# Performance work log

Hardware: AMD Instinct MI355X
Metric: run time of the kernel (lower is better)

The kernel has to match this reference:

```python
import jax, jax.numpy as jnp
import numpy as np
from jax import lax

D = 256      # d_model
NH = 4       # nhead == len(multi_size)
DH = D // NH # per-head dim = 64
B, H, W = 8, 32, 32
EPS_LN = 1e-5
EPS_ATT = 1e-6


def conv2d(x, w, pad):
    # x: [B,C,H,W], w: [O,I,k,k], SAME padding via pad=k//2
    return lax.conv_general_dilated(
        x, w, window_strides=(1, 1), padding=[(pad, pad), (pad, pad)],
        dimension_numbers=("NCHW", "OIHW", "NCHW"))


def layer_norm(x, g, b):
    m = jnp.mean(x, axis=-1, keepdims=True)
    v = jnp.mean((x - m) ** 2, axis=-1, keepdims=True)
    return (x - m) * lax.rsqrt(v + EPS_LN) * g + b


def setup_inputs() -> dict:
    key = jax.random.key(0)
    ks = jax.random.split(key, 20)
    s = 0.02
    inp = {
        "x": jax.random.normal(ks[0], (B, D, H, W), jnp.float32),
        "source": jax.random.normal(ks[1], (B, D, H, W), jnp.float32),
        # q projection: conv3x3 d_model -> d_model (bias-free)
        "Wq": jax.random.normal(ks[2], (D, D, 3, 3), jnp.float32) * s,
        # MultiConv k projection: kernels 1,3,5,7, each d_model -> dim
        "Wk1": jax.random.normal(ks[3], (DH, D, 1, 1), jnp.float32) * s,
        "Wk3": jax.random.normal(ks[4], (DH, D, 3, 3), jnp.float32) * s,
        "Wk5": jax.random.normal(ks[5], (DH, D, 5, 5), jnp.float32) * s,
        "Wk7": jax.random.normal(ks[6], (DH, D, 7, 7), jnp.float32) * s,
        # MultiConv v projection
        "Wv1": jax.random.normal(ks[7], (DH, D, 1, 1), jnp.float32) * s,
        "Wv3": jax.random.normal(ks[8], (DH, D, 3, 3), jnp.float32) * s,
        "Wv5": jax.random.normal(ks[9], (DH, D, 5, 5), jnp.float32) * s,
        "Wv7": jax.random.normal(ks[10], (DH, D, 7, 7), jnp.float32) * s,
        # merge linear (bias=False), stored [in,out]
        "Wm": jax.random.normal(ks[11], (D, D), jnp.float32) * s,
        "ln1_g": jnp.ones((D,), jnp.float32),
        "ln1_b": jnp.zeros((D,), jnp.float32),
        "ln2_g": jnp.ones((D,), jnp.float32),
        "ln2_b": jnp.zeros((D,), jnp.float32),
        # FF mlp: Linear(2D->2D, no bias), ReLU, Linear(2D->D, no bias); [in,out]
        "W1": jax.random.normal(ks[12], (2 * D, 2 * D), jnp.float32) * s,
        "W2": jax.random.normal(ks[13], (2 * D, D), jnp.float32) * s,
    }
    return inp


def _forward(x, source, Wq, Wk1, Wk3, Wk5, Wk7, Wv1, Wv3, Wv5, Wv7,
             Wm, ln1_g, ln1_b, ln2_g, ln2_b, W1, W2):
    b, c, h, w = x.shape
    h1, w1 = source.shape[2], source.shape[3]
    L = h * w
    S = h1 * w1

    # projections (multi-scale convs -> heads along channel)
    q = conv2d(x, Wq, 1)                                        # [b,D,h,w]
    k = jnp.concatenate([conv2d(source, Wk1, 0), conv2d(source, Wk3, 1),
                         conv2d(source, Wk5, 2), conv2d(source, Wk7, 3)], axis=1)
    v = jnp.concatenate([conv2d(source, Wv1, 0), conv2d(source, Wv3, 1),
                         conv2d(source, Wv5, 2), conv2d(source, Wv7, 3)], axis=1)

    # b c h w -> b (h w) (nhead dim) -> b L nhead dim
    q = q.transpose(0, 2, 3, 1).reshape(b, L, NH, DH)
    k = k.transpose(0, 2, 3, 1).reshape(b, S, NH, DH)
    v = v.transpose(0, 2, 3, 1).reshape(b, S, NH, DH)

    # FullAttention_vis: softmax attention map [b, L, S, nhead]
    temp = DH ** -0.5
    qk = jnp.einsum("blhd,bshd->blsh", q, k)
    attn_vis = jax.nn.softmax(qk * temp, axis=2)

    # LinearAttention (elu+1 kernel feature map)
    Qf = jax.nn.elu(q) + 1.0
    Kf = jax.nn.elu(k) + 1.0
    v_len = jnp.float32(S)
    vals = v / v_len
    KV = jnp.einsum("bshd,bshv->bhdv", Kf, vals)                # [b,NH,DH,DH]
    Z = 1.0 / (jnp.einsum("blhd,bhd->blh", Qf, Kf.sum(axis=1)) + EPS_ATT)
    msg = jnp.einsum("blhd,bhdv,blh->blhv", Qf, KV, Z) * v_len  # [b,L,NH,DH]

    # merge + norm1
    msg = layer_norm(msg.reshape(b, L, D) @ Wm, ln1_g, ln1_b)

    # FF (mlp): cat -> Linear -> ReLU -> Linear -> norm2
    xf = x.transpose(0, 2, 3, 1).reshape(b, L, c)
    ff = jax.nn.relu(jnp.concatenate([xf, msg], axis=2) @ W1) @ W2
    msg = layer_norm(ff, ln2_g, ln2_b)                          # [b,L,D]
    msg = msg.reshape(b, h, w, c).transpose(0, 3, 1, 2)         # b c h w

    out = x + msg
    # b (h0 w0) (h1 w1) c -> b c h0 w0 h1 w1
    vis = attn_vis.reshape(b, h, w, h1, w1, NH).transpose(0, 5, 1, 2, 3, 4)
    return out, vis


def reference(x, source, Wq, Wk1, Wk3, Wk5, Wk7, Wv1, Wv3, Wv5, Wv7,
              Wm, ln1_g, ln1_b, ln2_g, ln2_b, W1, W2):
    return _forward(x, source, Wq, Wk1, Wk3, Wk5, Wk7, Wv1, Wv3, Wv5, Wv7,
                    Wm, ln1_g, ln1_b, ln2_g, ln2_b, W1, W2)
```

## Files before the change

kernel.cpp:

```cpp
#include <hip/hip_runtime.h>

#define DEV __device__ __forceinline__

typedef unsigned short u16;
typedef unsigned int u32;
typedef __bf16 bf16x8 __attribute__((ext_vector_type(8)));
typedef float f32x4 __attribute__((ext_vector_type(4)));

DEV float elu1(float x) { return x > 0.f ? x + 1.f : __expf(x); }

DEV u16 f2bf(float f) {
    union { float f; unsigned u; } v; v.f = f;
    unsigned r = v.u + 0x7fffu + ((v.u >> 16) & 1u);
    return (u16)(r >> 16);
}

__global__ __launch_bounds__(256) void repack_kernel(
    const float* __restrict__ Wq,
    const float* __restrict__ Wk1, const float* __restrict__ Wk3,
    const float* __restrict__ Wk5, const float* __restrict__ Wk7,
    const float* __restrict__ Wv1, const float* __restrict__ Wv3,
    const float* __restrict__ Wv5, const float* __restrict__ Wv7,
    u16* __restrict__ wpack)
{
    int gid = blockIdx.x * 256 + threadIdx.x;
    int frag = gid >> 6, l = gid & 63;
    const float* W; int K, ocbase = 0, rel;
    if (frag < 1152) {
        W = Wq; K = 3; int slot = frag / 288; rel = frag % 288; ocbase = slot * 64;
    } else {
        int f = frag - 1152; int side = f / 2688; f %= 2688;
        if (f < 32)        { W = side ? Wv1 : Wk1; K = 1; rel = f; }
        else if (f < 320)  { W = side ? Wv3 : Wk3; K = 3; rel = f - 32; }
        else if (f < 1120) { W = side ? Wv5 : Wk5; K = 5; rel = f - 320; }
        else               { W = side ? Wv7 : Wk7; K = 7; rel = f - 1120; }
    }
    int og = rel & 3, cc = (rel >> 2) & 7, tap = rel >> 5;
    int dy = tap / K, dx = tap % K;
    int oc = ocbase + og * 16 + (l & 15);
    int c0 = cc * 32 + (l >> 4) * 8;
    u16 pk[8];
#pragma unroll
    for (int j = 0; j < 8; ++j)
        pk[j] = f2bf(W[((size_t)(oc * 256 + c0 + j) * K + dy) * K + dx]);
    *(int4*)&wpack[(size_t)frag * 512 + l * 8] = *(const int4*)pk;
}

__global__ __launch_bounds__(256) void cast_src_kernel(
    const float* __restrict__ x, const float* __restrict__ src,
    u16* __restrict__ xbh, u16* __restrict__ sbh)
{
    __shared__ float lds[32 * 129];
    const int i = blockIdx.x, t = threadIdx.x;
    const int inp = i >> 9, rem = i & 511;
    const int b = rem >> 6, cc = (rem >> 3) & 7, pxb = rem & 7;
    const float* in = (inp ? src : x) + ((size_t)b * 256 + cc * 32) * 1024 + pxb * 128;
    u16* outp = (inp ? sbh : xbh) + (size_t)b * 262144 + (size_t)cc * 32768 + pxb * 128 * 32;
#pragma unroll
    for (int u = 0; u < 4; ++u) {
        int unit = t + u * 256;
        int r = unit >> 5, px4 = unit & 31;
        float4 v = *(const float4*)(in + (size_t)r * 1024 + px4 * 4);
        lds[r * 129 + px4 * 4 + 0] = v.x;
        lds[r * 129 + px4 * 4 + 1] = v.y;
        lds[r * 129 + px4 * 4 + 2] = v.z;
        lds[r * 129 + px4 * 4 + 3] = v.w;
    }
    __syncthreads();
#pragma unroll
    for (int u = 0; u < 2; ++u) {
        int unit = t + u * 256;
        int px = unit >> 2, cg = unit & 3;
        u16 pk[8];
#pragma unroll
        for (int j = 0; j < 8; ++j) pk[j] = f2bf(lds[(cg * 8 + j) * 129 + px]);
        *(int4*)&outp[px * 32 + cg * 8] = *(const int4*)pk;
    }
}

__global__ __launch_bounds__(256) void cast_qk_kernel(
    const float* __restrict__ qb, const float* __restrict__ kb,
    u16* __restrict__ qbt, u16* __restrict__ kbt)
{
    __shared__ float lds[64 * 65];
    const int i = blockIdx.x, t = threadIdx.x;
    const int inp = i >> 9, rem = i & 511;
    const int b = rem >> 6, h = (rem >> 4) & 3, pxb = rem & 15;
    const float* in = (inp ? kb : qb) + ((size_t)b * 256 + h * 64) * 1024 + pxb * 64;
    u16* outp = (inp ? kbt : qbt) + (((size_t)(b * 4 + h)) * 1024 + pxb * 64) * 64;
#pragma unroll
    for (int u = 0; u < 4; ++u) {
        int unit = t + u * 256;
        int r = unit >> 4, px4 = unit & 15;
        float4 v = *(const float4*)(in + (size_t)r * 1024 + px4 * 4);
        lds[r * 65 + px4 * 4 + 0] = v.x;
        lds[r * 65 + px4 * 4 + 1] = v.y;
        lds[r * 65 + px4 * 4 + 2] = v.z;
        lds[r * 65 + px4 * 4 + 3] = v.w;
    }
    __syncthreads();
#pragma unroll
    for (int u = 0; u < 2; ++u) {
        int unit = t + u * 256;
        int px = unit >> 3, cg = unit & 7;
        u16 pk[8];
#pragma unroll
        for (int j = 0; j < 8; ++j) pk[j] = f2bf(lds[(cg * 8 + j) * 65 + px]);
        *(int4*)&outp[px * 64 + cg * 8] = *(const int4*)pk;
    }
}

__global__ __launch_bounds__(256) void repack_ff_kernel(
    const float* __restrict__ W1, const float* __restrict__ W2,
    u16* __restrict__ w1p, u16* __restrict__ w2p)
{
    int gid = blockIdx.x * 256 + threadIdx.x;
    int f = gid >> 6, l = gid & 63;
    u16 pk[8];
    if (f < 512) {
        int ks = f >> 5, nf = f & 31;
#pragma unroll
        for (int j = 0; j < 8; ++j)
            pk[j] = f2bf(W1[(size_t)(ks * 32 + (l >> 4) * 8 + j) * 512 + nf * 16 + (l & 15)]);
        *(int4*)&w1p[(size_t)f * 512 + l * 8] = *(const int4*)pk;
    } else {
        int f2 = f - 512;
        int ks = f2 >> 4, nf = f2 & 15;
#pragma unroll
        for (int j = 0; j < 8; ++j)
            pk[j] = f2bf(W2[(size_t)(ks * 32 + (l >> 4) * 8 + j) * 256 + nf * 16 + (l & 15)]);
        *(int4*)&w2p[(size_t)f2 * 512 + l * 8] = *(const int4*)pk;
    }
}

template<int K>
DEV void conv_mfma_body(const u16* __restrict__ srcb,
                        const u16* __restrict__ wsec,
                        float* __restrict__ dst,
                        u16* Bt, int y0, int cch0, int ncc, int t)
{
    constexpr int P = K / 2;
    const int w = t >> 6, l = t & 63;
    const int chi = l >> 4, ln = l & 15;
    const int rowbase = chi * 22 + w * 2 + 3 - P;
    const int colbase = ln + 3 - P;
    f32x4 acc[4][4];
#pragma unroll
    for (int m = 0; m < 4; ++m)
#pragma unroll
        for (int n = 0; n < 4; ++n) acc[m][n] = (f32x4){0.f, 0.f, 0.f, 0.f};

    for (int cc = 0; cc < ncc; ++cc) {
        const int ccg = cch0 + cc;
        __syncthreads();
#pragma unroll
        for (int u = 0; u < 7; ++u) {
            int unit = t + (u << 9);
            if (unit < 2816) {
                int xv = unit & 31, r = unit >> 5;
                int yy = r % 22, ch = r / 22;
                int ygl = y0 - 3 + yy;
                int4 pk;
                if ((unsigned)ygl < 32u)
                    pk = *(const int4*)&srcb[(size_t)ccg * 32768 + (ygl * 32 + xv) * 32 + ch * 8];
                else
                    pk = (int4){0, 0, 0, 0};
                *(int4*)&Bt[((ch * 22 + yy) * 40 + xv + 3) * 8] = pk;
            } else if (unit < 3520) {
                int hu = unit - 2816;
                int hx = hu & 7; int xi = hx < 3 ? hx : hx + 32;
                int r = hu >> 3; int yy = r % 22, ch = r / 22;
                int4 z = {0, 0, 0, 0};
                *(int4*)&Bt[((ch * 22 + yy) * 40 + xi) * 8] = z;
            }
        }
        __syncthreads();
#pragma unroll
        for (int dy = 0; dy < K; ++dy) {
#pragma unroll
            for (int dx = 0; dx < K; ++dx) {
                const int tap = dy * K + dx;
                const u16* wp = wsec + ((size_t)(tap * 8 + ccg) * 4) * 512 + l * 8;
                bf16x8 a0 = *(const bf16x8*)(wp);
                bf16x8 a1 = *(const bf16x8*)(wp + 512);
                bf16x8 a2 = *(const bf16x8*)(wp + 1024);
                bf16x8 a3 = *(const bf16x8*)(wp + 1536);
                bf16x8 bf[4];
#pragma unroll
                for (int n = 0; n < 4; ++n) {
                    int row = rowbase + dy + (n >> 1);
                    int col = colbase + dx + (n & 1) * 16;
                    bf[n] = *(const bf16x8*)&Bt[(row * 40 + col) * 8];
                }
#pragma unroll
                for (int n = 0; n < 4; ++n) {
                    acc[0][n] = __builtin_amdgcn_mfma_f32_16x16x32_bf16(a0, bf[n], acc[0][n], 0, 0, 0);
                    acc[1][n] = __builtin_amdgcn_mfma_f32_16x16x32_bf16(a1, bf[n], acc[1][n], 0, 0, 0);
                    acc[2][n] = __builtin_amdgcn_mfma_f32_16x16x32_bf16(a2, bf[n], acc[2][n], 0, 0, 0);
                    acc[3][n] = __builtin_amdgcn_mfma_f32_16x16x32_bf16(a3, bf[n], acc[3][n], 0, 0, 0);
                }
            }
        }
    }
#pragma unroll
    for (int m = 0; m < 4; ++m)
#pragma unroll
        for (int n = 0; n < 4; ++n) {
            int y = y0 + w * 2 + (n >> 1);
            int px = y * 32 + (n & 1) * 16 + ln;
            int ocb = m * 16 + chi * 4;
#pragma unroll
            for (int r = 0; r < 4; ++r)
                dst[(size_t)(ocb + r) * 1024 + px] = acc[m][n][r];
        }
}

__global__ __launch_bounds__(512) void conv_mfma_kernel(
    const u16* __restrict__ xbh, const u16* __restrict__ sbh,
    const u16* __restrict__ wpack,
    float* __restrict__ qb, float* __restrict__ kb, float* __restrict__ vb,
    float* __restrict__ p5, float* __restrict__ p7)
{
    __shared__ u16 Bt[4 * 22 * 40 * 8];
    const int bx = blockIdx.x, t = threadIdx.x;
    const int b = bx >> 6, r = bx & 63;
    if (r < 8) {
        int slot = r >> 1, yt = r & 1;
        conv_mfma_body<3>(xbh + (size_t)b * 262144,
                          wpack + (size_t)(slot * 288) * 512,
                          qb + ((size_t)b * 256 + slot * 64) * 1024,
                          Bt, yt * 16, 0, 8, t);
        return;
    }
    const int r2 = r - 8;
    const int side = r2 / 28, r3 = r2 % 28;
    const u16* sp = sbh + (size_t)b * 262144;
    float* fin = side ? vb : kb;
    const size_t wkb = 1152 + (size_t)side * 2688;
    if (r3 < 2) {
        conv_mfma_body<1>(sp, wpack + (wkb + 0) * 512,
                          fin + ((size_t)b * 256) * 1024, Bt, r3 * 16, 0, 8, t);
    } else if (r3 < 4) {
        conv_mfma_body<3>(sp, wpack + (wkb + 32) * 512,
                          fin + ((size_t)b * 256 + 64) * 1024, Bt, (r3 - 2) * 16, 0, 8, t);
    } else if (r3 < 12) {
        int t5 = r3 - 4, cpart = t5 >> 1, yt = t5 & 1;
        conv_mfma_body<5>(sp, wpack + (wkb + 320) * 512,
                          p5 + (((size_t)side * 4 + cpart) * 8 + b) * 65536,
                          Bt, yt * 16, cpart * 2, 2, t);
    } else {
        int t7 = r3 - 12, cpart = t7 >> 1, yt = t7 & 1;
        conv_mfma_body<7>(sp, wpack + (wkb + 1120) * 512,
                          p7 + (((size_t)side * 8 + cpart) * 8 + b) * 65536,
                          Bt, yt * 16, cpart, 1, t);
    }
}

__global__ __launch_bounds__(256) void reduce_kernel(
    const float* __restrict__ p5, const float* __restrict__ p7,
    float* __restrict__ kb, float* __restrict__ vb)
{
    int gid = blockIdx.x * 256 + threadIdx.x;
    int px4 = gid & 255;
    int rr = gid >> 8;
    int oc = rr & 63, b = (rr >> 6) & 7, head = (rr >> 9) & 1, side = rr >> 10;
    float* outb = side ? vb : kb;
    float4 s = make_float4(0.f, 0.f, 0.f, 0.f);
    if (head == 0) {
#pragma unroll
        for (int p = 0; p < 4; ++p) {
            float4 u = *((const float4*)(p5 + (((size_t)side * 4 + p) * 8 + b) * 65536 + (size_t)oc * 1024) + px4);
            s.x += u.x; s.y += u.y; s.z += u.z; s.w += u.w;
        }
        *((float4*)(outb + ((size_t)b * 256 + 128 + oc) * 1024) + px4) = s;
    } else {
#pragma unroll
        for (int p = 0; p < 8; ++p) {
            float4 u = *((const float4*)(p7 + (((size_t)side * 8 + p) * 8 + b) * 65536 + (size_t)oc * 1024) + px4);
            s.x += u.x; s.y += u.y; s.z += u.z; s.w += u.w;
        }
        *((float4*)(outb + ((size_t)b * 256 + 192 + oc) * 1024) + px4) = s;
    }
}

__global__ __launch_bounds__(512) void qk_sm_kernel(const u16* __restrict__ qbt,
                                                    const u16* __restrict__ kbt,
                                                    float* __restrict__ vis)
{
    __shared__ u16 kf[32 * 512];
    __shared__ u16 qf[4 * 512];
    __shared__ float redM[32 * 8];
    __shared__ float redS[32 * 8];
    const int t = threadIdx.x;
    const int bx = blockIdx.x;
    const int b = bx >> 7, h = (bx >> 5) & 3, l0 = (bx & 31) * 32;
    const u16* qtp = qbt + ((size_t)(b * 4 + h)) * 1024 * 64;
    const u16* ktp = kbt + ((size_t)(b * 4 + h)) * 1024 * 64;

    if (t < 256) {
        int r = t & 31, dblk = t >> 5;
        int4 pk = *(const int4*)&qtp[(size_t)(l0 + r) * 64 + dblk * 8];
        *(int4*)&qf[(((r >> 4) * 2 + (dblk >> 2)) * 64 + (dblk & 3) * 16 + (r & 15)) * 8] = pk;
    }
    __syncthreads();

    const int w = t >> 6, l = t & 63, ln = l & 15, lg = l >> 4;
    bf16x8 a[2][2];
#pragma unroll
    for (int fr = 0; fr < 2; ++fr)
#pragma unroll
        for (int ks = 0; ks < 2; ++ks)
            a[fr][ks] = *(const bf16x8*)&qf[((fr * 2 + ks) * 64 + l) * 8];

    f32x4 acc[2][4][2];
#pragma unroll
    for (int fr = 0; fr < 2; ++fr)
#pragma unroll
        for (int cc = 0; cc < 4; ++cc)
#pragma unroll
            for (int f = 0; f < 2; ++f) acc[fr][cc][f] = (f32x4){0.f, 0.f, 0.f, 0.f};

#pragma unroll
    for (int cc = 0; cc < 4; ++cc) {
        __syncthreads();
#pragma unroll
        for (int it = 0; it < 4; ++it) {
            int unit = it * 512 + t;
            int sl = unit & 255, dblk = unit >> 8;
            int4 pk = *(const int4*)&ktp[(size_t)(cc * 256 + sl) * 64 + dblk * 8];
            *(int4*)&kf[(((sl >> 4) * 2 + (dblk >> 2)) * 64 + (dblk & 3) * 16 + (sl & 15)) * 8] = pk;
        }
        __syncthreads();
#pragma unroll
        for (int f = 0; f < 2; ++f) {
            int fg = (w * 2 + f) * 2;
            bf16x8 b0 = *(const bf16x8*)&kf[((fg + 0) * 64 + l) * 8];
            bf16x8 b1 = *(const bf16x8*)&kf[((fg + 1) * 64 + l) * 8];
#pragma unroll
            for (int fr = 0; fr < 2; ++fr) {
                acc[fr][cc][f] = __builtin_amdgcn_mfma_f32_16x16x32_bf16(a[fr][0], b0, acc[fr][cc][f], 0, 0, 0);
                acc[fr][cc][f] = __builtin_amdgcn_mfma_f32_16x16x32_bf16(a[fr][1], b1, acc[fr][cc][f], 0, 0, 0);
            }
        }
    }

#pragma unroll
    for (int fr = 0; fr < 2; ++fr)
#pragma unroll
        for (int cc = 0; cc < 4; ++cc)
#pragma unroll
            for (int f = 0; f < 2; ++f)
#pragma unroll
                for (int e = 0; e < 4; ++e) acc[fr][cc][f][e] *= 0.125f;

    float rmax[2][4];
#pragma unroll
    for (int fr = 0; fr < 2; ++fr)
#pragma unroll
        for (int reg = 0; reg < 4; ++reg) {
            float m = -1e30f;
#pragma unroll
            for (int cc = 0; cc < 4; ++cc)
#pragma unroll
                for (int f = 0; f < 2; ++f) m = fmaxf(m, acc[fr][cc][f][reg]);
#pragma unroll
            for (int off = 1; off < 16; off <<= 1) m = fmaxf(m, __shfl_xor(m, off));
            if (ln == 0) redM[(fr * 16 + lg * 4 + reg) * 8 + w] = m;
            rmax[fr][reg] = m;
        }
    __syncthreads();
#pragma unroll
    for (int fr = 0; fr < 2; ++fr)
#pragma unroll
        for (int reg = 0; reg < 4; ++reg) {
            int r = fr * 16 + lg * 4 + reg;
            float m = redM[r * 8];
#pragma unroll
            for (int ww = 1; ww < 8; ++ww) m = fmaxf(m, redM[r * 8 + ww]);
            rmax[fr][reg] = m;
        }
#pragma unroll
    for (int fr = 0; fr < 2; ++fr)
#pragma unroll
        for (int reg = 0; reg < 4; ++reg) {
            float s = 0.f;
            float m = rmax[fr][reg];
#pragma unroll
            for (int cc = 0; cc < 4; ++cc)
#pragma unroll
                for (int f = 0; f < 2; ++f) {
                    float e = __expf(acc[fr][cc][f][reg] - m);
                    acc[fr][cc][f][reg] = e;
                    s += e;
                }
#pragma unroll
            for (int off = 1; off < 16; off <<= 1) s += __shfl_xor(s, off);
            if (ln == 0) redS[(fr * 16 + lg * 4 + reg) * 8 + w] = s;
        }
    __syncthreads();
    float* visp = vis + (((size_t)(b * 4 + h)) << 20);
#pragma unroll
    for (int fr = 0; fr < 2; ++fr)
#pragma unroll
        for (int reg = 0; reg < 4; ++reg) {
            int r = fr * 16 + lg * 4 + reg;
            float s = redS[r * 8] + redS[r * 8 + 1] + redS[r * 8 + 2] + redS[r * 8 + 3]
                    + redS[r * 8 + 4] + redS[r * 8 + 5] + redS[r * 8 + 6] + redS[r * 8 + 7];
            float inv = 1.f / s;
            float* vr = visp + (size_t)(l0 + r) * 1024 + w * 32 + ln;
#pragma unroll
            for (int cc = 0; cc < 4; ++cc)
#pragma unroll
                for (int f = 0; f < 2; ++f)
                    vr[cc * 256 + f * 16] = acc[fr][cc][f][reg] * inv;
        }
}

__global__ __launch_bounds__(256) void kv_kernel(const float* __restrict__ k,
                                                 const float* __restrict__ v,
                                                 float* __restrict__ KVp,
                                                 float* __restrict__ Ksump)
{
    __shared__ float4 Kt4[64*17];
    __shared__ float4 Vt4[64*16];
    float* Kt = (float*)Kt4;
    float* Vt = (float*)Vt4;
    const int t = threadIdx.x;
    const int bx = blockIdx.x;
    const int b = bx >> 4, h = (bx >> 2) & 3, ch = bx & 3;
    const float* kb = k + ((size_t)b*256 + h*64)*1024 + ch*256;
    const float* vb = v + ((size_t)b*256 + h*64)*1024 + ch*256;
    const int d = t >> 2, v0 = (t & 3) * 16;
    float4 acc[4];
#pragma unroll
    for (int j = 0; j < 4; ++j) acc[j] = make_float4(0.f, 0.f, 0.f, 0.f);
    float ks = 0.f;
    for (int st = 0; st < 4; ++st) {
        __syncthreads();
        {
            int dd = t >> 2, r0 = (t & 3) * 16;
#pragma unroll
            for (int mm = 0; mm < 4; ++mm) {
                float4 kv = *(const float4*)(kb + dd*1024 + st*64 + r0 + mm*4);
                Kt[(r0+mm*4+0)*68 + dd] = elu1(kv.x);
                Kt[(r0+mm*4+1)*68 + dd] = elu1(kv.y);
                Kt[(r0+mm*4+2)*68 + dd] = elu1(kv.z);
                Kt[(r0+mm*4+3)*68 + dd] = elu1(kv.w);
                float4 vv = *(const float4*)(vb + dd*1024 + st*64 + r0 + mm*4);
                Vt[(r0+mm*4+0)*64 + dd] = vv.x;
                Vt[(r0+mm*4+1)*64 + dd] = vv.y;
                Vt[(r0+mm*4+2)*64 + dd] = vv.z;
                Vt[(r0+mm*4+3)*64 + dd] = vv.w;
            }
        }
        __syncthreads();
#pragma unroll 8
        for (int s = 0; s < 64; ++s) {
            float kf = Kt[s*68 + d];
            const float4* vp = (const float4*)(Vt + s*64 + v0);
#pragma unroll
            for (int j = 0; j < 4; ++j) {
                float4 vv = vp[j];
                acc[j].x += kf*vv.x; acc[j].y += kf*vv.y;
                acc[j].z += kf*vv.z; acc[j].w += kf*vv.w;
            }
        }
        if (t < 64) {
#pragma unroll 8
            for (int s = 0; s < 64; ++s) ks += Kt[s*68 + t];
        }
    }
    float* op = KVp + ((size_t)((ch*32 + b*4 + h)*64 + d))*64 + v0;
#pragma unroll
    for (int j = 0; j < 4; ++j) ((float4*)op)[j] = acc[j];
    if (t < 64) Ksump[(size_t)(ch*32 + b*4 + h)*64 + t] = ks;
}

__global__ __launch_bounds__(256) void msg_kernel(const float* __restrict__ q,
                                                  const float* __restrict__ KVp,
                                                  const float* __restrict__ Ksump,
                                                  float* __restrict__ msg)
{
    __shared__ float4 kvl4[4*1028];
    __shared__ float ksl[4*65];
    float* kvl = (float*)kvl4;
    const int t = threadIdx.x;
    const int bx = blockIdx.x;
    const int b = bx >> 4;
    const int l0 = (bx & 15) * 64;
    for (int m = 0; m < 64; ++m) {
        int idx = t + 256*m;
        int hh = idx >> 12, dd = (idx >> 6) & 63, vv = idx & 63;
        float s = 0.f;
#pragma unroll
        for (int ch = 0; ch < 4; ++ch)
            s += KVp[(size_t)((ch*32 + b*4))*4096 + idx];
        kvl[hh*4112 + dd*64 + vv] = s;
    }
    {
        float s = 0.f;
#pragma unroll
        for (int ch = 0; ch < 4; ++ch)
            s += Ksump[(size_t)(ch*32 + b*4)*64 + t];
        ksl[(t >> 6)*65 + (t & 63)] = s;
    }
    __syncthreads();
    const int h = t & 3, l = l0 + (t >> 2);
    const float* qb = q + ((size_t)b*256 + h*64)*1024 + l;
    float qf[64];
#pragma unroll
    for (int dd = 0; dd < 64; ++dd) qf[dd] = elu1(qb[dd*1024]);
    float zd = 1e-6f;
#pragma unroll
    for (int dd = 0; dd < 64; ++dd) zd += qf[dd] * ksl[h*65 + dd];
    const float Z = 1.f / zd;
    float* op = msg + ((size_t)(b*1024 + l))*256 + h*64;
    for (int c0 = 0; c0 < 64; c0 += 16) {
        float4 a[4];
#pragma unroll
        for (int j = 0; j < 4; ++j) a[j] = make_float4(0.f, 0.f, 0.f, 0.f);
#pragma unroll
        for (int dd = 0; dd < 64; ++dd) {
            float qv = qf[dd];
            const float4* kp = (const float4*)(kvl + h*4112 + dd*64 + c0);
#pragma unroll
            for (int j = 0; j < 4; ++j) {
                float4 kk = kp[j];
                a[j].x += qv*kk.x; a[j].y += qv*kk.y;
                a[j].z += qv*kk.z; a[j].w += qv*kk.w;
            }
        }
#pragma unroll
        for (int j = 0; j < 4; ++j) {
            a[j].x *= Z; a[j].y *= Z; a[j].z *= Z; a[j].w *= Z;
            ((float4*)(op + c0))[j] = a[j];
        }
    }
}

__global__ __launch_bounds__(256) void merge_ln1_kernel(const float* __restrict__ msg,
                                                        const float* __restrict__ Wm,
                                                        const float* __restrict__ g1,
                                                        const float* __restrict__ b1,
                                                        float* __restrict__ msgm)
{
    __shared__ float4 mL4[16*65];
    __shared__ float mv[32];
    float* mL = (float*)mL4;
    const int t = threadIdx.x;
    const size_t base = (size_t)blockIdx.x * 16;
    {
        int r = t >> 4, cb = t & 15;
#pragma unroll
        for (int j = 0; j < 16; ++j)
            mL[r*260 + cb + 16*j] = msg[(base + r)*256 + cb + 16*j];
    }
    __syncthreads();
    float acc[16];
#pragma unroll
    for (int r = 0; r < 16; ++r) acc[r] = 0.f;
    for (int i = 0; i < 256; i += 4) {
        float w0 = Wm[(size_t)(i+0)*256 + t];
        float w1 = Wm[(size_t)(i+1)*256 + t];
        float w2 = Wm[(size_t)(i+2)*256 + t];
        float w3 = Wm[(size_t)(i+3)*256 + t];
#pragma unroll
        for (int r = 0; r < 16; ++r) {
            float4 m4 = mL4[r*65 + (i >> 2)];
            acc[r] += m4.x*w0 + m4.y*w1 + m4.z*w2 + m4.w*w3;
        }
    }
    __syncthreads();
#pragma unroll
    for (int r = 0; r < 16; ++r) mL[r*260 + t] = acc[r];
    __syncthreads();
    {
        int wid = t >> 6, lane = t & 63;
#pragma unroll
        for (int rr = 0; rr < 4; ++rr) {
            int r = wid*4 + rr;
            float s1 = 0.f, s2 = 0.f;
#pragma unroll
            for (int m = 0; m < 4; ++m) {
                float vv = mL[r*260 + lane + 64*m];
                s1 += vv; s2 += vv*vv;
            }
#pragma unroll
            for (int off = 1; off < 64; off <<= 1) {
                s1 += __shfl_xor(s1, off);
                s2 += __shfl_xor(s2, off);
            }
            if (lane == 0) {
                float mean = s1 * (1.f/256.f);
                float var  = s2 * (1.f/256.f) - mean*mean;
                mv[r*2]   = mean;
                mv[r*2+1] = rsqrtf(var + 1e-5f);
            }
        }
    }
    __syncthreads();
    const float gg = g1[t], bb = b1[t];
#pragma unroll
    for (int r = 0; r < 16; ++r) {
        float val = (mL[r*260 + t] - mv[r*2]) * mv[r*2+1] * gg + bb;
        msgm[(base + r)*256 + t] = val;
    }
}

__global__ __launch_bounds__(256) void ff_mfma_kernel(
    const float* __restrict__ x, const float* __restrict__ msgm,
    const u16* __restrict__ w1p, const u16* __restrict__ w2p,
    const float* __restrict__ g2, const float* __restrict__ b2,
    float* __restrict__ out)
{
    __shared__ u16 tile[32 * 520];
    __shared__ float redS[32 * 4];
    __shared__ float redQ[32 * 4];
    float* tf = (float*)tile;
    const int t = threadIdx.x;
    const int base = blockIdx.x * 32;
    const int b = base >> 10, l0 = base & 1023;
    const int w = t >> 6, l = t & 63, ln = l & 15, lg = l >> 4;

    {
        int rr = t & 31, cg = t >> 5;
        for (int cci = 0; cci < 32; ++cci) {
            int c = cci * 8 + cg;
            float v = x[((size_t)b * 256 + c) * 1024 + l0 + rr];
            tile[rr * 520 + c] = f2bf(v);
        }
        int r = t >> 3, cb = (t & 7) * 32;
#pragma unroll
        for (int i = 0; i < 8; ++i) {
            float4 v = *(const float4*)&msgm[((size_t)(base + r)) * 256 + cb + i * 4];
            u32 p0 = (u32)f2bf(v.x) | ((u32)f2bf(v.y) << 16);
            u32 p1 = (u32)f2bf(v.z) | ((u32)f2bf(v.w) << 16);
            *(u32*)&tile[r * 520 + 256 + cb + i * 4] = p0;
            *(u32*)&tile[r * 520 + 256 + cb + i * 4 + 2] = p1;
        }
    }
    __syncthreads();

    f32x4 acc[2][8];
#pragma unroll
    for (int fr = 0; fr < 2; ++fr)
#pragma unroll
        for (int fc = 0; fc < 8; ++fc) acc[fr][fc] = (f32x4){0.f, 0.f, 0.f, 0.f};
    for (int ks = 0; ks < 16; ++ks) {
        bf16x8 a0 = *(const bf16x8*)&tile[(ln) * 520 + ks * 32 + lg * 8];
        bf16x8 a1 = *(const bf16x8*)&tile[(16 + ln) * 520 + ks * 32 + lg * 8];
#pragma unroll
        for (int fc = 0; fc < 8; ++fc) {
            bf16x8 bb = *(const bf16x8*)&w1p[((size_t)(ks * 32 + w * 8 + fc) * 64 + l) * 8];
            acc[0][fc] = __builtin_amdgcn_mfma_f32_16x16x32_bf16(a0, bb, acc[0][fc], 0, 0, 0);
            acc[1][fc] = __builtin_amdgcn_mfma_f32_16x16x32_bf16(a1, bb, acc[1][fc], 0, 0, 0);
        }
    }
    __syncthreads();
#pragma unroll
    for (int fr = 0; fr < 2; ++fr)
#pragma unroll
        for (int fc = 0; fc < 8; ++fc)
#pragma unroll
            for (int reg = 0; reg < 4; ++reg) {
                int r = fr * 16 + lg * 4 + reg;
                int c = w * 128 + fc * 16 + ln;
                tile[r * 520 + c] = f2bf(fmaxf(acc[fr][fc][reg], 0.f));
            }
    __syncthreads();

    f32x4 acc2[2][4];
#pragma unroll
    for (int fr = 0; fr < 2; ++fr)
#pragma unroll
        for (int fc = 0; fc < 4; ++fc) acc2[fr][fc] = (f32x4){0.f, 0.f, 0.f, 0.f};
    for (int ks = 0; ks < 16; ++ks) {
        bf16x8 a0 = *(const bf16x8*)&tile[(ln) * 520 + ks * 32 + lg * 8];
        bf16x8 a1 = *(const bf16x8*)&tile[(16 + ln) * 520 + ks * 32 + lg * 8];
#pragma unroll
        for (int fc = 0; fc < 4; ++fc) {
            bf16x8 bb = *(const bf16x8*)&w2p[((size_t)(ks * 16 + w * 4 + fc) * 64 + l) * 8];
            acc2[0][fc] = __builtin_amdgcn_mfma_f32_16x16x32_bf16(a0, bb, acc2[0][fc], 0, 0, 0);
            acc2[1][fc] = __builtin_amdgcn_mfma_f32_16x16x32_bf16(a1, bb, acc2[1][fc], 0, 0, 0);
        }
    }
#pragma unroll
    for (int fr = 0; fr < 2; ++fr)
#pragma unroll
        for (int reg = 0; reg < 4; ++reg) {
            float s = 0.f, qsum = 0.f;
#pragma unroll
            for (int fc = 0; fc < 4; ++fc) {
                float v = acc2[fr][fc][reg];
                s += v; qsum += v * v;
            }
#pragma unroll
            for (int off = 1; off < 16; off <<= 1) {
                s += __shfl_xor(s, off);
                qsum += __shfl_xor(qsum, off);
            }
            if (ln == 0) {
                int r = fr * 16 + lg * 4 + reg;
                redS[r * 4 + w] = s;
                redQ[r * 4 + w] = qsum;
            }
        }
    __syncthreads();
    float mean[2][4], rstd[2][4];
#pragma unroll
    for (int fr = 0; fr < 2; ++fr)
#pragma unroll
        for (int reg = 0; reg < 4; ++reg) {
            int r = fr * 16 + lg * 4 + reg;
            float s = redS[r * 4] + redS[r * 4 + 1] + redS[r * 4 + 2] + redS[r * 4 + 3];
            float qs = redQ[r * 4] + redQ[r * 4 + 1] + redQ[r * 4 + 2] + redQ[r * 4 + 3];
            float m = s * (1.f / 256.f);
            mean[fr][reg] = m;
            rstd[fr][reg] = rsqrtf(qs * (1.f / 256.f) - m * m + 1e-5f);
        }
#pragma unroll
    for (int fc = 0; fc < 4; ++fc) {
        int c = w * 64 + fc * 16 + ln;
        float gg = g2[c], bb = b2[c];
#pragma unroll
        for (int fr = 0; fr < 2; ++fr)
#pragma unroll
            for (int reg = 0; reg < 4; ++reg) {
                int r = fr * 16 + lg * 4 + reg;
                tf[r * 260 + c] = (acc2[fr][fc][reg] - mean[fr][reg]) * rstd[fr][reg] * gg + bb;
            }
    }
    __syncthreads();
    {
        const float* xp = x + ((size_t)b * 256 + t) * 1024 + l0;
        float* op = out + ((size_t)b * 256 + t) * 1024 + l0;
#pragma unroll
        for (int i = 0; i < 8; ++i) {
            float4 xv = *(const float4*)(xp + i * 4);
            float4 o;
            o.x = xv.x + tf[(i * 4 + 0) * 260 + t];
            o.y = xv.y + tf[(i * 4 + 1) * 260 + t];
            o.z = xv.z + tf[(i * 4 + 2) * 260 + t];
            o.w = xv.w + tf[(i * 4 + 3) * 260 + t];
            *(float4*)(op + i * 4) = o;
        }
    }
}

extern "C" void kernel_launch(void* const* d_in, const int* in_sizes, int n_in,
                              void* d_out, int out_size, void* d_ws, size_t ws_size,
                              hipStream_t stream)
{
    const float* x    = (const float*)d_in[0];
    const float* src  = (const float*)d_in[1];
    const float* Wq   = (const float*)d_in[2];
    const float* Wk1  = (const float*)d_in[3];
    const float* Wk3  = (const float*)d_in[4];
    const float* Wk5  = (const float*)d_in[5];
    const float* Wk7  = (const float*)d_in[6];
    const float* Wv1  = (const float*)d_in[7];
    const float* Wv3  = (const float*)d_in[8];
    const float* Wv5  = (const float*)d_in[9];
    const float* Wv7  = (const float*)d_in[10];
    const float* Wm   = (const float*)d_in[11];
    const float* g1   = (const float*)d_in[12];
    const float* b1   = (const float*)d_in[13];
    const float* g2   = (const float*)d_in[14];
    const float* b2   = (const float*)d_in[15];
    const float* W1   = (const float*)d_in[16];
    const float* W2   = (const float*)d_in[17];

    float* out = (float*)d_out;
    float* vis = out + 2097152;

    float* p5 = vis;
    float* p7 = vis + 4194304;

    float* ws    = (float*)d_ws;
    float* qb    = ws;
    float* kb    = ws + 2097152;
    float* vb    = ws + 4194304;
    u16*   wpack = (u16*)(ws + 6291456);
    u16*   w1p   = (u16*)(ws + 6291456);
    u16*   w2p   = (u16*)(ws + 6422528);
    u16*   qbt   = (u16*)(ws + 6488064);
    u16*   kbt   = (u16*)(ws + 7536640);
    u16*   xbh   = (u16*)(ws + 7962624);
    u16*   sbh   = (u16*)(ws + 9011200);
    float* msg   = ws + 7962624;
    float* msgm  = ws + 10059776;
    float* KVp   = ws + 12156928;
    float* Ksump = ws + 12681216;

    repack_kernel   <<<1632, 256, 0, stream>>>(Wq, Wk1, Wk3, Wk5, Wk7,
                                               Wv1, Wv3, Wv5, Wv7, wpack);
    cast_src_kernel <<<1024, 256, 0, stream>>>(x, src, xbh, sbh);
    conv_mfma_kernel<<<512,  512, 0, stream>>>(xbh, sbh, wpack, qb, kb, vb, p5, p7);
    reduce_kernel   <<<2048, 256, 0, stream>>>(p5, p7, kb, vb);
    repack_ff_kernel<<<192,  256, 0, stream>>>(W1, W2, w1p, w2p);
    cast_qk_kernel  <<<1024, 256, 0, stream>>>(qb, kb, qbt, kbt);
    qk_sm_kernel    <<<1024, 512, 0, stream>>>(qbt, kbt, vis);
    kv_kernel       <<<128,  256, 0, stream>>>(kb, vb, KVp, Ksump);
    msg_kernel      <<<128,  256, 0, stream>>>(qb, KVp, Ksump, msg);
    merge_ln1_kernel<<<512,  256, 0, stream>>>(msg, Wm, g1, b1, msgm);
    ff_mfma_kernel  <<<256,  256, 0, stream>>>(x, msgm, w1p, w2p, g2, b2, out);
}
```

Before: 308.8 us.

## Prefetch next input channel chunk into registers and remap conv block grid

After: 372.8 us. 20.7% more time.

```diff
diff --git a/kernel.cpp b/kernel.cpp
--- a/kernel.cpp
+++ b/kernel.cpp
@@ -133,6 +133,49 @@
     }
 }
 
+DEV void stage_load4(const u16* __restrict__ srcb, int ccg, int y0, int t, int4* pk)
+{
+#pragma unroll
+    for (int u = 0; u < 4; ++u) {
+        int unit = t + (u << 9);
+        int xv = unit & 31, r = unit >> 5;
+        int yy = r % 22, ch = r / 22;
+        int ygl = y0 - 3 + yy;
+        int4 v = {0, 0, 0, 0};
+        if ((unsigned)ygl < 32u)
+            v = *(const int4*)&srcb[(size_t)ccg * 32768 + (ygl * 32 + xv) * 32 + ch * 8];
+        pk[u] = v;
+    }
+}
+
+DEV void stage_write(u16* Bt, const u16* __restrict__ srcb, int ccg, int y0,
+                     int t, const int4* pk)
+{
+#pragma unroll
+    for (int u = 0; u < 7; ++u) {
+        int unit = t + (u << 9);
+        if (unit < 2816) {
+            int xv = unit & 31, r = unit >> 5;
+            int yy = r % 22, ch = r / 22;
+            int4 v;
+            if (u < 4) v = pk[u];
+            else {
+                int ygl = y0 - 3 + yy;
+                v = (int4){0, 0, 0, 0};
+                if ((unsigned)ygl < 32u)
+                    v = *(const int4*)&srcb[(size_t)ccg * 32768 + (ygl * 32 + xv) * 32 + ch * 8];
+            }
+            *(int4*)&Bt[((ch * 22 + yy) * 40 + xv + 3) * 8] = v;
+        } else if (unit < 3520) {
+            int hu = unit - 2816;
+            int hx = hu & 7; int xi = hx < 3 ? hx : hx + 32;
+            int r = hu >> 3; int yy = r % 22, ch = r / 22;
+            int4 z = {0, 0, 0, 0};
+            *(int4*)&Bt[((ch * 22 + yy) * 40 + xi) * 8] = z;
+        }
+    }
+}
+
 template<int K>
 DEV void conv_mfma_body(const u16* __restrict__ srcb,
                         const u16* __restrict__ wsec,
@@ -150,31 +193,15 @@
 #pragma unroll
         for (int n = 0; n < 4; ++n) acc[m][n] = (f32x4){0.f, 0.f, 0.f, 0.f};
 
+    int4 pk[4];
+    stage_load4(srcb, cch0, y0, t, pk);
+
     for (int cc = 0; cc < ncc; ++cc) {
         const int ccg = cch0 + cc;
         __syncthreads();
-#pragma unroll
-        for (int u = 0; u < 7; ++u) {
-            int unit = t + (u << 9);
-            if (unit < 2816) {
-                int xv = unit & 31, r = unit >> 5;
-                int yy = r % 22, ch = r / 22;
-                int ygl = y0 - 3 + yy;
-                int4 pk;
-                if ((unsigned)ygl < 32u)
-                    pk = *(const int4*)&srcb[(size_t)ccg * 32768 + (ygl * 32 + xv) * 32 + ch * 8];
-                else
-                    pk = (int4){0, 0, 0, 0};
-                *(int4*)&Bt[((ch * 22 + yy) * 40 + xv + 3) * 8] = pk;
-            } else if (unit < 3520) {
-                int hu = unit - 2816;
-                int hx = hu & 7; int xi = hx < 3 ? hx : hx + 32;
-                int r = hu >> 3; int yy = r % 22, ch = r / 22;
-                int4 z = {0, 0, 0, 0};
-                *(int4*)&Bt[((ch * 22 + yy) * 40 + xi) * 8] = z;
-            }
-        }
+        stage_write(Bt, srcb, ccg, y0, t, pk);
         __syncthreads();
+        if (cc + 1 < ncc) stage_load4(srcb, ccg + 1, y0, t, pk);
 #pragma unroll
         for (int dy = 0; dy < K; ++dy) {
 #pragma unroll
@@ -215,7 +242,7 @@
         }
 }
 
-__global__ __launch_bounds__(512) void conv_mfma_kernel(
+__global__ __launch_bounds__(512, 4) void conv_mfma_kernel(
     const u16* __restrict__ xbh, const u16* __restrict__ sbh,
     const u16* __restrict__ wpack,
     float* __restrict__ qb, float* __restrict__ kb, float* __restrict__ vb,
@@ -223,36 +250,35 @@
 {
     __shared__ u16 Bt[4 * 22 * 40 * 8];
     const int bx = blockIdx.x, t = threadIdx.x;
-    const int b = bx >> 6, r = bx & 63;
-    if (r < 8) {
-        int slot = r >> 1, yt = r & 1;
+    const int g = bx & 31, b = (bx >> 5) & 7, m = bx >> 8;
+    if (g < 4) {
         conv_mfma_body<3>(xbh + (size_t)b * 262144,
-                          wpack + (size_t)(slot * 288) * 512,
-                          qb + ((size_t)b * 256 + slot * 64) * 1024,
-                          Bt, yt * 16, 0, 8, t);
+                          wpack + (size_t)(g * 288) * 512,
+                          qb + ((size_t)b * 256 + g * 64) * 1024,
+                          Bt, m * 16, 0, 8, t);
         return;
     }
-    const int r2 = r - 8;
-    const int side = r2 / 28, r3 = r2 % 28;
+    const int gs = g - 4;
+    const int side = gs / 14, gg = gs % 14;
     const u16* sp = sbh + (size_t)b * 262144;
     float* fin = side ? vb : kb;
     const size_t wkb = 1152 + (size_t)side * 2688;
-    if (r3 < 2) {
+    if (gg == 0) {
         conv_mfma_body<1>(sp, wpack + (wkb + 0) * 512,
-                          fin + ((size_t)b * 256) * 1024, Bt, r3 * 16, 0, 8, t);
-    } else if (r3 < 4) {
+                          fin + ((size_t)b * 256) * 1024, Bt, m * 16, 0, 8, t);
+    } else if (gg == 1) {
         conv_mfma_body<3>(sp, wpack + (wkb + 32) * 512,
-                          fin + ((size_t)b * 256 + 64) * 1024, Bt, (r3 - 2) * 16, 0, 8, t);
-    } else if (r3 < 12) {
-        int t5 = r3 - 4, cpart = t5 >> 1, yt = t5 & 1;
+                          fin + ((size_t)b * 256 + 64) * 1024, Bt, m * 16, 0, 8, t);
+    } else if (gg < 6) {
+        int cpart = gg - 2;
         conv_mfma_body<5>(sp, wpack + (wkb + 320) * 512,
                           p5 + (((size_t)side * 4 + cpart) * 8 + b) * 65536,
-                          Bt, yt * 16, cpart * 2, 2, t);
+                          Bt, m * 16, cpart * 2, 2, t);
     } else {
-        int t7 = r3 - 12, cpart = t7 >> 1, yt = t7 & 1;
+        int cpart = gg - 6;
         conv_mfma_body<7>(sp, wpack + (wkb + 1120) * 512,
                           p7 + (((size_t)side * 8 + cpart) * 8 + b) * 65536,
-                          Bt, yt * 16, cpart, 1, t);
+                          Bt, m * 16, cpart, 1, t);
     }
 }
 
```
